# Kernel optimization log

Hardware: AMD Instinct MI355X
Metric: run time of the kernel (lower is better)

## Reference

```python
import jax, jax.numpy as jnp
import numpy as np

LMAX, MMAX = 4, 2
K = (LMAX + 1) ** 2                                 # 25 SH coefficients (l-major node layout)
NL = [LMAX - m + 1 for m in range(MMAX + 1)]        # coeffs per order m: [5,4,3]
M_COEFF = NL[0] + sum(2 * n for n in NL[1:])        # 19 coeffs in m-major (mmax-truncated) edge layout
SPHERE_C, HIDDEN_C = 64, 64
NUM_HEADS, ALPHA_C, VALUE_C, OUT_C = 8, 32, 16, 64
P_GRID = 100
N_NODES, N_EDGES = 4096, 24576
NUM_SPECIES, EDGE_C, EMB_C = 90, 64, 64
N_EXTRA = NUM_HEADS * ALPHA_C + HIDDEN_C            # extra m=0 channels for S2_SEP: alpha + gate scalars


def _ln(x, g, b, eps=1e-5):
    mu = jnp.mean(x, -1, keepdims=True)
    var = jnp.var(x, -1, keepdims=True)
    return (x - mu) * jax.lax.rsqrt(var + eps) * g + b


def _smooth_leaky_relu(x, neg=0.2):
    return 0.5 * (1.0 + neg) * x + 0.5 * (1.0 - neg) * x * (2.0 * jax.nn.sigmoid(x) - 1.0)


def _segment_softmax(a, seg, n):
    amax = jax.lax.stop_gradient(jax.ops.segment_max(a, seg, num_segments=n))
    amax = jnp.where(jnp.isfinite(amax), amax, 0.0)
    e = jnp.exp(a - amax[seg])
    s = jax.ops.segment_sum(e, seg, num_segments=n)
    return e / (s[seg] + 1e-16)


def _so2_conv(x, w0, b0, wms, c_in, c_out, x_edge=None, n_extra=0):
    # x: [E, M_COEFF, c_in] in m-major layout (m=0 block, then per m: real rows then imag rows)
    E = x.shape[0]
    L0 = NL[0]
    x0 = x[:, :L0, :].reshape(E, L0 * c_in)
    if x_edge is not None:
        x0 = x0 * x_edge[:, :L0 * c_in]
    y0 = x0 @ w0 + b0
    extra = None
    if n_extra:
        extra = y0[:, L0 * c_out:]
        y0 = y0[:, :L0 * c_out]
    outs = [y0.reshape(E, L0, c_out)]
    off, rad = L0, L0 * c_in
    for m in range(1, MMAX + 1):
        nl = NL[m]
        xr = x[:, off:off + nl, :]
        xi = x[:, off + nl:off + 2 * nl, :]
        if x_edge is not None:
            s = x_edge[:, rad:rad + nl * c_in].reshape(E, nl, c_in)
            xr, xi = xr * s, xi * s
        xr = xr.reshape(E, nl * c_in)
        xi = xi.reshape(E, nl * c_in)
        half = nl * c_out
        wa, wb = wms[m - 1][:, :half], wms[m - 1][:, half:]
        yr = (xr @ wa - xi @ wb).reshape(E, nl, c_out)  # complex block-matmul
        yi = (xr @ wb + xi @ wa).reshape(E, nl, c_out)
        outs.append(jnp.concatenate([yr, yi], axis=1))
        off += 2 * nl
        rad += nl * c_in
    return jnp.concatenate(outs, axis=1), extra


def setup_inputs():
    key = jax.random.key(0)
    ks = iter(jax.random.split(key, 48))
    def w(shape, fan_in):
        return jax.random.normal(next(ks), shape, jnp.float32) / np.sqrt(fan_in)
    inp = {}
    inp['node_feats'] = jax.random.normal(next(ks), (N_NODES, K, SPHERE_C), jnp.float32)
    inp['node_species'] = jax.random.randint(next(ks), (N_NODES,), 0, NUM_SPECIES)
    inp['edge_distances'] = jax.random.normal(next(ks), (N_EDGES, EDGE_C), jnp.float32)
    inp['senders'] = jax.random.randint(next(ks), (N_EDGES,), 0, N_NODES)
    inp['receivers'] = jax.random.randint(next(ks), (N_EDGES,), 0, N_NODES)
    inp['wigner'] = jax.random.normal(next(ks), (N_EDGES, M_COEFF, K), jnp.float32) / np.sqrt(K)
    inp['snd_emb'] = jax.random.normal(next(ks), (NUM_SPECIES, EMB_C), jnp.float32) * 0.001
    inp['rcv_emb'] = jax.random.normal(next(ks), (NUM_SPECIES, EMB_C), jnp.float32) * 0.001
    ec = EDGE_C + 2 * EMB_C                              # 192 after atom-edge embedding concat
    n_rad = 2 * SPHERE_C * (NL[0] + NL[1] + NL[2])       # 1536 per-edge scales for conv1
    inp['rad_w1'] = w((ec, 64), ec); inp['rad_b1'] = jnp.zeros((64,))
    inp['rad_g1'] = jnp.ones((64,)); inp['rad_be1'] = jnp.zeros((64,))
    inp['rad_w2'] = w((64, 64), 64); inp['rad_b2'] = jnp.zeros((64,))
    inp['rad_g2'] = jnp.ones((64,)); inp['rad_be2'] = jnp.zeros((64,))
    inp['rad_w3'] = w((64, n_rad), 64); inp['rad_b3'] = jnp.ones((n_rad,))
    cin1 = 2 * SPHERE_C
    inp['c1_w0'] = w((NL[0] * cin1, NL[0] * HIDDEN_C + N_EXTRA), NL[0] * cin1)
    inp['c1_b0'] = jnp.zeros((NL[0] * HIDDEN_C + N_EXTRA,))
    inp['c1_wm1'] = w((NL[1] * cin1, 2 * NL[1] * HIDDEN_C), NL[1] * cin1)
    inp['c1_wm2'] = w((NL[2] * cin1, 2 * NL[2] * HIDDEN_C), NL[2] * cin1)
    inp['aln_g'] = jnp.ones((ALPHA_C,)); inp['aln_b'] = jnp.zeros((ALPHA_C,))
    inp['alpha_dot'] = w((NUM_HEADS, ALPHA_C), ALPHA_C)
    inp['to_grid'] = jax.random.normal(next(ks), (P_GRID, M_COEFF), jnp.float32) / np.sqrt(M_COEFF)
    inp['from_grid'] = jax.random.normal(next(ks), (M_COEFF, P_GRID), jnp.float32) / np.sqrt(P_GRID)
    cv = NUM_HEADS * VALUE_C
    inp['c2_w0'] = w((NL[0] * HIDDEN_C, NL[0] * cv), NL[0] * HIDDEN_C)
    inp['c2_b0'] = jnp.zeros((NL[0] * cv,))
    inp['c2_wm1'] = w((NL[1] * HIDDEN_C, 2 * NL[1] * cv), NL[1] * HIDDEN_C)
    inp['c2_wm2'] = w((NL[2] * HIDDEN_C, 2 * NL[2] * cv), NL[2] * HIDDEN_C)
    inp['proj_w'] = w((LMAX + 1, cv, OUT_C), cv)
    inp['proj_b'] = jnp.zeros((OUT_C,))
    return inp


def reference(node_feats, node_species, edge_distances, senders, receivers, wigner,
              snd_emb, rcv_emb, rad_w1, rad_b1, rad_g1, rad_be1, rad_w2, rad_b2,
              rad_g2, rad_be2, rad_w3, rad_b3, c1_w0, c1_b0, c1_wm1, c1_wm2,
              aln_g, aln_b, alpha_dot, to_grid, from_grid,
              c2_w0, c2_b0, c2_wm1, c2_wm2, proj_w, proj_b):
    N = node_feats.shape[0]
    # atom-edge embedding gathers + concat with radial-basis distances
    edge_embeds = jnp.concatenate([edge_distances,
                                   snd_emb[node_species[senders]],
                                   rcv_emb[node_species[receivers]]], axis=1)
    msgs = jnp.concatenate([node_feats[senders], node_feats[receivers]], axis=2)  # [E,25,128]
    msgs = jnp.einsum('emk,ekc->emc', wigner, msgs)                               # rotate to edge frame [E,19,128]
    # radial function -> per-edge input scales for SO2 conv 1
    h = jax.nn.silu(_ln(edge_embeds @ rad_w1 + rad_b1, rad_g1, rad_be1))
    h = jax.nn.silu(_ln(h @ rad_w2 + rad_b2, rad_g2, rad_be2))
    x_edge = h @ rad_w3 + rad_b3
    msgs, x0_extra = _so2_conv(msgs, c1_w0, c1_b0, [c1_wm1, c1_wm2],
                               2 * SPHERE_C, HIDDEN_C, x_edge, N_EXTRA)
    x0_alpha = x0_extra[:, :NUM_HEADS * ALPHA_C]
    x0_gate = x0_extra[:, NUM_HEADS * ALPHA_C:]
    # separable S2 activation: SiLU on sphere grid for l>0, SiLU on scalars for l=0
    grid = jax.nn.silu(jnp.einsum('pm,emc->epc', to_grid, msgs))
    tens = jnp.einsum('mp,epc->emc', from_grid, grid)
    msgs = jnp.concatenate([jax.nn.silu(x0_gate)[:, None, :], tens[:, 1:, :]], axis=1)
    msgs, _ = _so2_conv(msgs, c2_w0, c2_b0, [c2_wm1, c2_wm2], HIDDEN_C, NUM_HEADS * VALUE_C)
    # attention weights: LN -> SmoothLeakyReLU -> dot -> per-receiver softmax
    a = _smooth_leaky_relu(_ln(x0_alpha.reshape(-1, NUM_HEADS, ALPHA_C), aln_g, aln_b))
    alpha = _segment_softmax(jnp.einsum('ehk,hk->eh', a, alpha_dot), receivers, N)
    attn = msgs.reshape(-1, M_COEFF, NUM_HEADS, VALUE_C) * alpha[:, None, :, None]
    msgs = attn.reshape(-1, M_COEFF, NUM_HEADS * VALUE_C)
    msgs = jnp.einsum('emk,emc->ekc', wigner, msgs)    # rotate back (W^T), [E,25,128]
    node = jax.ops.segment_sum(msgs, receivers, num_segments=N)
    # SO3 linear: per-degree-l channel mixing, bias only on l=0
    l_of_k = jnp.asarray(np.repeat(np.arange(LMAX + 1), 2 * np.arange(LMAX + 1) + 1))
    out = jnp.einsum('nkc,kcd->nkd', node, proj_w[l_of_k])
    return out.at[:, 0, :].add(proj_b)
```

## Files before the change

kernel.cpp:

```cpp
#include <hip/hip_runtime.h>

typedef unsigned short u16;
typedef unsigned int u32;
typedef __attribute__((ext_vector_type(8))) short short8;
typedef __attribute__((ext_vector_type(4))) float floatx4;

#define E_EDGES 24576
#define EC 12288
#define N_NODES_C 4096

__device__ __forceinline__ float bf2f(u16 u) {
    union { u32 i; float f; } v; v.i = ((u32)u) << 16; return v.f;
}
__device__ __forceinline__ u16 f2bf(float f) {
    union { float f; u32 i; } v; v.f = f;
    u32 x = v.i;
    u32 r = (x + 0x7fffu + ((x >> 16) & 1u)) >> 16;
    return (u16)r;
}
__device__ __forceinline__ u32 pk_bf16(float a, float b) {
    u32 r;
    asm("v_cvt_pk_bf16_f32 %0, %1, %2" : "=v"(r) : "v"(a), "v"(b));
    return r;
}
__device__ __forceinline__ u32 encf(float f) {
    union { float f; u32 i; } v; v.f = f;
    return (v.i & 0x80000000u) ? ~v.i : (v.i | 0x80000000u);
}
__device__ __forceinline__ float decf(u32 u) {
    union { u32 i; float f; } v;
    v.i = (u & 0x80000000u) ? (u ^ 0x80000000u) : ~u;
    return v.f;
}
__device__ __forceinline__ float sigmoidf_(float x) { return __fdividef(1.f, 1.f + __expf(-x)); }
__device__ __forceinline__ float siluf_(float x) { return x * __fdividef(1.f, 1.f + __expf(-x)); }

__device__ __forceinline__ void gld16(const u16* g, u16* l) {
    __builtin_amdgcn_global_load_lds((const __attribute__((address_space(1))) unsigned int*)g,
                                     (__attribute__((address_space(3))) unsigned int*)l, 16, 0, 0);
}

__global__ void k_diag(float* __restrict__ out, int n) {
    int i = blockIdx.x * 256 + threadIdx.x;
    if (i < n) out[i] = 1000.0f;
}

__global__ void k_transpose(const float* __restrict__ src, u16* __restrict__ dst, int K, int N) {
    int idx = blockIdx.x * 256 + threadIdx.x;
    if (idx >= K * N) return;
    int k = idx / N, n = idx % N;
    dst[n * K + k] = f2bf(src[idx]);
}
__global__ void k_combine(const float* __restrict__ src, u16* __restrict__ dst, int K, int H) {
    int total = 4 * K * H;
    int idx = blockIdx.x * 256 + threadIdx.x;
    if (idx >= total) return;
    int n = idx / (2 * K), k = idx % (2 * K);
    float v;
    if (k < K) v = src[k * 2 * H + n];
    else {
        int kk = k - K;
        if (n < H) v = -src[kk * 2 * H + H + n];
        else       v = src[kk * 2 * H + (n - H)];
    }
    dst[idx] = f2bf(v);
}

__global__ void k_packgrid(const float* __restrict__ tg, const float* __restrict__ fg,
                           u16* __restrict__ tgP, u16* __restrict__ fgP) {
    int idx = blockIdx.x * 256 + threadIdx.x;
    if (idx < 112 * 32) {
        int p = idx >> 5, m = idx & 31;
        tgP[idx] = (p < 100 && m < 19) ? f2bf(tg[p * 19 + m]) : (u16)0;
    }
    int j = idx - 112 * 32;
    if (j >= 0 && j < 32 * 128) {
        int m = j >> 7, k = j & 127;
        fgP[j] = (m < 19 && k < 100) ? f2bf(fg[m * 100 + k]) : (u16)0;
    }
}

__global__ void k_init(u32* __restrict__ nmax, float* __restrict__ nsum, int n) {
    int idx = blockIdx.x * 256 + threadIdx.x;
    if (idx < n) { nmax[idx] = 0x007FFFFFu;  nsum[idx] = 0.f; }
}

__global__ void k_deg(const int* __restrict__ rcv, u32* __restrict__ deg) {
    int e = blockIdx.x * 256 + threadIdx.x;
    if (e < E_EDGES) atomicAdd(&deg[rcv[e]], 1u);
}
__global__ __launch_bounds__(256) void k_pfx(const u32* __restrict__ deg,
                                             u32* __restrict__ rowstart, u32* __restrict__ cur) {
    __shared__ u32 ps[256];
    int t = threadIdx.x;
    u32 loc[16]; u32 s = 0;
#pragma unroll
    for (int i = 0; i < 16; i++) { loc[i] = s; s += deg[t * 16 + i]; }
    ps[t] = s;
    __syncthreads();
    for (int o = 1; o < 256; o <<= 1) {
        u32 v = (t >= o) ? ps[t - o] : 0u;
        __syncthreads();
        ps[t] += v;
        __syncthreads();
    }
    u32 base = (t == 0) ? 0u : ps[t - 1];
#pragma unroll
    for (int i = 0; i < 16; i++) { u32 v = base + loc[i]; rowstart[t * 16 + i] = v; cur[t * 16 + i] = v; }
}
__global__ void k_fill(const int* __restrict__ rcv, u32* __restrict__ cur, int* __restrict__ elist) {
    int e = blockIdx.x * 256 + threadIdx.x;
    if (e < E_EDGES) { u32 p = atomicAdd(&cur[rcv[e]], 1u); elist[p] = e; }
}

__global__ void k_ee(const float* __restrict__ dist, const int* __restrict__ species,
                     const int* __restrict__ snd, const int* __restrict__ rcv,
                     const float* __restrict__ semb, const float* __restrict__ remb,
                     u16* __restrict__ ee) {
    int idx = blockIdx.x * 256 + threadIdx.x;
    if (idx >= E_EDGES * 192) return;
    int e = idx / 192, c = idx % 192;
    float v;
    if (c < 64)       v = dist[e * 64 + c];
    else if (c < 128) v = semb[species[snd[e]] * 64 + (c - 64)];
    else              v = remb[species[rcv[e]] * 64 + (c - 128)];
    ee[idx] = f2bf(v);
}

__global__ __launch_bounds__(256) void k_gemm(
    const u16* __restrict__ A, int lda,
    const u16* __restrict__ BT, int ldb,
    u16* __restrict__ C, int ldc,
    int N, int K,
    const float* __restrict__ bias) {
    __shared__ u16 As[128 * 32];
    __shared__ u16 Bs[128 * 32];
    int tid = threadIdx.x;
    int bm0 = blockIdx.x * 128;
    int bn0 = blockIdx.y * 128;
    int wave = tid >> 6, lane = tid & 63;
    int wm = (wave >> 1) * 64, wn = (wave & 1) * 64;
    int lrow = lane & 15, lk = (lane >> 4) * 8;

    int srow = (wave << 4) + (lane >> 2);
    int schunk = (lane & 3) << 3;
    const u16* Arow0 = A + (size_t)(bm0 + srow) * lda + schunk;
    const u16* Arow1 = A + (size_t)(bm0 + srow + 64) * lda + schunk;
    int n0 = bn0 + srow;      if (n0 >= N) n0 = N - 1;
    int n1 = bn0 + srow + 64; if (n1 >= N) n1 = N - 1;
    const u16* Brow0 = BT + (size_t)n0 * ldb + schunk;
    const u16* Brow1 = BT + (size_t)n1 * ldb + schunk;
    u16* lA0 = &As[srow * 32 + schunk];
    u16* lA1 = &As[(srow + 64) * 32 + schunk];
    u16* lB0 = &Bs[srow * 32 + schunk];
    u16* lB1 = &Bs[(srow + 64) * 32 + schunk];

    floatx4 acc[4][4];
#pragma unroll
    for (int i = 0; i < 4; i++)
#pragma unroll
        for (int j = 0; j < 4; j++) acc[i][j] = floatx4{0.f, 0.f, 0.f, 0.f};

    for (int k0 = 0; k0 < K; k0 += 32) {
        gld16(Arow0 + k0, lA0);
        gld16(Arow1 + k0, lA1);
        gld16(Brow0 + k0, lB0);
        gld16(Brow1 + k0, lB1);
        asm volatile("s_waitcnt vmcnt(0)" ::: "memory");
        __syncthreads();
        short8 a[4], b[4];
#pragma unroll
        for (int i = 0; i < 4; i++) a[i] = *(const short8*)(&As[(wm + i * 16 + lrow) * 32 + lk]);
#pragma unroll
        for (int j = 0; j < 4; j++) b[j] = *(const short8*)(&Bs[(wn + j * 16 + lrow) * 32 + lk]);
#pragma unroll
        for (int i = 0; i < 4; i++)
#pragma unroll
            for (int j = 0; j < 4; j++)
                acc[i][j] = __builtin_amdgcn_mfma_f32_16x16x32_bf16(b[j], a[i], acc[i][j], 0, 0, 0);
        __syncthreads();
    }

    int q = lane >> 4;
#pragma unroll
    for (int i = 0; i < 4; i++) {
        int row = bm0 + wm + i * 16 + lrow;
#pragma unroll
        for (int j = 0; j < 4; j++) {
            int col = bn0 + wn + j * 16 + q * 4;
            if (col < N) {
                float4 bv = bias ? *(const float4*)(&bias[col]) : float4{0.f, 0.f, 0.f, 0.f};
                uint2 pv;
                pv.x = pk_bf16(acc[i][j][0] + bv.x, acc[i][j][1] + bv.y);
                pv.y = pk_bf16(acc[i][j][2] + bv.z, acc[i][j][3] + bv.w);
                *(uint2*)(&C[(size_t)row * ldc + col]) = pv;
            }
        }
    }
}

__global__ __launch_bounds__(256) void k_ln_silu(const u16* __restrict__ in, u16* __restrict__ out,
                                                 const float* __restrict__ g, const float* __restrict__ b) {
    int tid = threadIdx.x;
    int e = blockIdx.x * 4 + (tid >> 6);
    int c = tid & 63;
    float x = bf2f(in[(size_t)e * 64 + c]);
    float s = x, s2 = x * x;
#pragma unroll
    for (int o = 32; o; o >>= 1) { s += __shfl_xor(s, o); s2 += __shfl_xor(s2, o); }
    float mu = s * (1.f / 64.f);
    float var = s2 * (1.f / 64.f) - mu * mu;
    float rs = rsqrtf(var + 1e-5f);
    float y = (x - mu) * rs * g[c] + b[c];
    out[(size_t)e * 64 + c] = f2bf(siluf_(y));
}

__global__ __launch_bounds__(256) void k_rotate(const float* __restrict__ nf, const float* __restrict__ wig,
                                                const int* __restrict__ snd, const int* __restrict__ rcv,
                                                const u16* __restrict__ xe, u16* __restrict__ A1, int e0) {
    __shared__ float wl[2][475];
    int tid = threadIdx.x;
    for (int i = tid; i < 950; i += 256) {
        int ee = e0 + blockIdx.x * 2 + (i / 475);
        wl[i / 475][i % 475] = wig[(size_t)ee * 475 + (i % 475)];
    }
    __syncthreads();
    int le = tid >> 7, c = tid & 127;
    int el = blockIdx.x * 2 + le;
    int e = e0 + el;
    int nd = (c < 64) ? snd[e] : rcv[e];
    int cc = c & 63;
    float msg[25];
#pragma unroll
    for (int k = 0; k < 25; k++) msg[k] = nf[(size_t)nd * 1600 + k * 64 + cc];
    const float* w = wl[le];
    size_t ebase = (size_t)el * 2432;
    size_t xbase = (size_t)el * 1536;
#pragma unroll
    for (int m = 0; m < 19; m++) {
        float r = 0.f;
#pragma unroll
        for (int k = 0; k < 25; k++) r += w[m * 25 + k] * msg[k];
        int a1c, xc;
        if (m < 5)       { a1c = m * 128;               xc = m * 128; }
        else if (m < 9)  { a1c = 640 + (m - 5) * 128;   xc = 640 + (m - 5) * 128; }
        else if (m < 13) { a1c = 1152 + (m - 9) * 128;  xc = 640 + (m - 9) * 128; }
        else if (m < 16) { a1c = 1664 + (m - 13) * 128; xc = 1152 + (m - 13) * 128; }
        else             { a1c = 2048 + (m - 16) * 128; xc = 1152 + (m - 16) * 128; }
        float sc = bf2f(xe[xbase + xc + c]);
        A1[ebase + a1c + c] = f2bf(r * sc);
    }
}

__global__ __launch_bounds__(256) void k_logits(const u16* __restrict__ Y0, const int* __restrict__ rcv,
                                                const float* __restrict__ g, const float* __restrict__ b,
                                                const float* __restrict__ adot,
                                                float* __restrict__ logits, u32* __restrict__ nmax) {
    int e = blockIdx.x;
    int tid = threadIdx.x;
    int h = tid >> 5, c = tid & 31;
    float x = bf2f(Y0[(size_t)e * 640 + 320 + h * 32 + c]);
    float s = x, s2 = x * x;
#pragma unroll
    for (int o = 16; o; o >>= 1) { s += __shfl_xor(s, o); s2 += __shfl_xor(s2, o); }
    float mu = s * (1.f / 32.f);
    float var = s2 * (1.f / 32.f) - mu * mu;
    float rs = rsqrtf(var + 1e-5f);
    float a = (x - mu) * rs * g[c] + b[c];
    float f = 0.6f * a + 0.4f * a * (2.f * sigmoidf_(a) - 1.f);
    float l = f * adot[h * 32 + c];
#pragma unroll
    for (int o = 16; o; o >>= 1) l += __shfl_xor(l, o);
    if (c == 0) {
        logits[e * 8 + h] = l;
        atomicMax(&nmax[rcv[e] * 8 + h], encf(l));
    }
}

__global__ void k_expsum(const float* __restrict__ logits, const int* __restrict__ rcv,
                         const u32* __restrict__ nmax, float* __restrict__ ealpha, float* __restrict__ nsum) {
    int idx = blockIdx.x * 256 + threadIdx.x;
    if (idx >= E_EDGES * 8) return;
    int e = idx >> 3, h = idx & 7;
    int r = rcv[e];
    float amax = decf(nmax[r * 8 + h]);
    if (!(amax > -1e38f && amax < 1e38f)) amax = 0.f;
    float v = __expf(logits[idx] - amax);
    ealpha[idx] = v;
    atomicAdd(&nsum[r * 8 + h], v);
}

#define GR_XS_STR 40
#define GR_T1_STR 136
__global__ __launch_bounds__(256) void k_grid_mfma(
    const u16* __restrict__ Y0, const u16* __restrict__ Y1, const u16* __restrict__ Y2,
    const u16* __restrict__ tgP, const u16* __restrict__ fgP, u16* __restrict__ A2) {
    __shared__ u16 T1s[128 * GR_T1_STR];
    u16* Xs = T1s;
    int tid = threadIdx.x;
    int e0 = blockIdx.x * 2;
    {
        int mp = tid & 15;
        int c0 = ((tid >> 4) & 7) << 3;
        int le = tid >> 7;
        int e = e0 + le;
        int m0 = 2 * mp, m1 = m0 + 1;
        uint4 va = {0, 0, 0, 0}, vb = {0, 0, 0, 0};
        if (m0 < 5)       va = *(const uint4*)(&Y0[(size_t)e * 640 + m0 * 64 + c0]);
        else if (m0 < 13) va = *(const uint4*)(&Y1[(size_t)e * 512 + (m0 - 5) * 64 + c0]);
        else if (m0 < 19) va = *(const uint4*)(&Y2[(size_t)e * 384 + (m0 - 13) * 64 + c0]);
        if (m1 < 5)       vb = *(const uint4*)(&Y0[(size_t)e * 640 + m1 * 64 + c0]);
        else if (m1 < 13) vb = *(const uint4*)(&Y1[(size_t)e * 512 + (m1 - 5) * 64 + c0]);
        else if (m1 < 19) vb = *(const uint4*)(&Y2[(size_t)e * 384 + (m1 - 13) * 64 + c0]);
        const u16* pa = (const u16*)&va;
        const u16* pb = (const u16*)&vb;
        int rbase = le * 64 + c0;
#pragma unroll
        for (int j = 0; j < 8; j++) {
            u32 w = (u32)pa[j] | ((u32)pb[j] << 16);
            *(u32*)(&Xs[(rbase + j) * GR_XS_STR + 2 * mp]) = w;
        }
    }
    __syncthreads();
    int wave = tid >> 6, lane = tid & 63;
    int wn = wave << 5;
    int ln = lane & 15, q = lane >> 4;
    short8 bx0 = *(const short8*)(&Xs[(wn + ln) * GR_XS_STR + q * 8]);
    short8 bx1 = *(const short8*)(&Xs[(wn + 16 + ln) * GR_XS_STR + q * 8]);
    floatx4 acc1[2][7];
#pragma unroll
    for (int pt = 0; pt < 7; pt++) {
        short8 a = *(const short8*)(&tgP[(size_t)(pt * 16 + ln) * 32 + q * 8]);
        acc1[0][pt] = __builtin_amdgcn_mfma_f32_16x16x32_bf16(a, bx0, floatx4{0.f, 0.f, 0.f, 0.f}, 0, 0, 0);
        acc1[1][pt] = __builtin_amdgcn_mfma_f32_16x16x32_bf16(a, bx1, floatx4{0.f, 0.f, 0.f, 0.f}, 0, 0, 0);
    }
    __syncthreads();
    {
        int row = tid >> 1;
        uint4 z = {0, 0, 0, 0};
        *(uint4*)(&T1s[row * GR_T1_STR + 112 + (tid & 1) * 8]) = z;
    }
#pragma unroll
    for (int i = 0; i < 2; i++) {
        u16* dst = &T1s[(wn + i * 16 + ln) * GR_T1_STR + q * 4];
#pragma unroll
        for (int pt = 0; pt < 7; pt++) {
            uint2 pv;
            pv.x = pk_bf16(siluf_(acc1[i][pt][0]), siluf_(acc1[i][pt][1]));
            pv.y = pk_bf16(siluf_(acc1[i][pt][2]), siluf_(acc1[i][pt][3]));
            *(uint2*)(dst + pt * 16) = pv;
        }
    }
    __syncthreads();
    floatx4 acc2[2][2];
    acc2[0][0] = floatx4{0.f, 0.f, 0.f, 0.f}; acc2[0][1] = floatx4{0.f, 0.f, 0.f, 0.f};
    acc2[1][0] = floatx4{0.f, 0.f, 0.f, 0.f}; acc2[1][1] = floatx4{0.f, 0.f, 0.f, 0.f};
#pragma unroll
    for (int ks = 0; ks < 4; ks++) {
        short8 c0 = *(const short8*)(&T1s[(wn + ln) * GR_T1_STR + ks * 32 + q * 8]);
        short8 c1 = *(const short8*)(&T1s[(wn + 16 + ln) * GR_T1_STR + ks * 32 + q * 8]);
#pragma unroll
        for (int ct = 0; ct < 2; ct++) {
            short8 b = *(const short8*)(&fgP[(size_t)(ct * 16 + ln) * 128 + ks * 32 + q * 8]);
            acc2[0][ct] = __builtin_amdgcn_mfma_f32_16x16x32_bf16(c0, b, acc2[0][ct], 0, 0, 0);
            acc2[1][ct] = __builtin_amdgcn_mfma_f32_16x16x32_bf16(c1, b, acc2[1][ct], 0, 0, 0);
        }
    }
#pragma unroll
    for (int rt = 0; rt < 2; rt++) {
        int row = wn + rt * 16 + q * 4;
        int e = e0 + (row >> 6), c = row & 63;
#pragma unroll
        for (int ct = 0; ct < 2; ct++) {
            int mp = ct * 16 + ln;
            if (mp >= 1 && mp < 19) {
                uint2 pv;
                pv.x = pk_bf16(acc2[rt][ct][0], acc2[rt][ct][1]);
                pv.y = pk_bf16(acc2[rt][ct][2], acc2[rt][ct][3]);
                *(uint2*)(&A2[(size_t)e * 1216 + mp * 64 + c]) = pv;
            }
        }
    }
    if (tid < 128) {
        int e = e0 + (tid >> 6), c = tid & 63;
        float gate = bf2f(Y0[(size_t)e * 640 + 576 + c]);
        A2[(size_t)e * 1216 + c] = f2bf(siluf_(gate));
    }
}

__global__ __launch_bounds__(256) void k_gather(
    const u16* __restrict__ Z0, const u16* __restrict__ Z1, const u16* __restrict__ Z2,
    const float* __restrict__ wig, const float* __restrict__ ealpha, const float* __restrict__ nsum,
    const u32* __restrict__ rowstart, const u32* __restrict__ deg, const int* __restrict__ elist,
    float* __restrict__ node, int e0, int accum) {
    int n = blockIdx.x * 4 + (threadIdx.x >> 6);
    int lane = threadIdx.x & 63;
    int h = lane >> 3;
    float sden = __fdividef(1.f, nsum[n * 8 + h] + 1e-16f);
    float a0[25], a1[25];
#pragma unroll
    for (int k = 0; k < 25; k++) { a0[k] = 0.f; a1[k] = 0.f; }
    u32 lo = rowstart[n], cnt = deg[n];
    bool did = false;
    for (u32 i = 0; i < cnt; i++) {
        int e = __builtin_amdgcn_readfirstlane(elist[lo + i]);
        int el = e - e0;
        if ((u32)el >= (u32)EC) continue;
        did = true;
        float al = ealpha[e * 8 + h] * sden;
        u32 zp[19];
        const u16* z0 = Z0 + (size_t)el * 640 + 2 * lane;
        const u16* z1 = Z1 + (size_t)el * 1024 + 2 * lane;
        const u16* z2 = Z2 + (size_t)el * 768 + 2 * lane;
#pragma unroll
        for (int m = 0; m < 5; m++) zp[m] = *(const u32*)(z0 + m * 128);
#pragma unroll
        for (int m = 0; m < 8; m++) zp[5 + m] = *(const u32*)(z1 + m * 128);
#pragma unroll
        for (int m = 0; m < 6; m++) zp[13 + m] = *(const u32*)(z2 + m * 128);
        const float* __restrict__ w = wig + (size_t)e * 475;
#pragma unroll
        for (int m = 0; m < 19; m++) {
            float s0 = bf2f((u16)(zp[m] & 0xffffu)) * al;
            float s1 = bf2f((u16)(zp[m] >> 16)) * al;
#pragma unroll
            for (int k = 0; k < 25; k++) {
                float wv = w[m * 25 + k];
                a0[k] = fmaf(wv, s0, a0[k]);
                a1[k] = fmaf(wv, s1, a1[k]);
            }
        }
    }
    float* nb = node + (size_t)n * 3200 + 2 * lane;
    if (accum) {
        if (!did) return;
#pragma unroll
        for (int k = 0; k < 25; k++) {
            float2 v = *(float2*)(&nb[k * 128]);
            v.x += a0[k]; v.y += a1[k];
            *(float2*)(&nb[k * 128]) = v;
        }
    } else {
#pragma unroll
        for (int k = 0; k < 25; k++) {
            float2 v; v.x = a0[k]; v.y = a1[k];
            *(float2*)(&nb[k * 128]) = v;
        }
    }
}

#define PJ_STR 136
__global__ __launch_bounds__(256) void k_proj_mfma(
    const float* __restrict__ node, const u16* __restrict__ pwTb,
    const float* __restrict__ pb, float* __restrict__ out) {
    __shared__ u16 As[128 * PJ_STR];
    __shared__ u16 Bs[64 * PJ_STR];
    int tid = threadIdx.x;
    int n0 = blockIdx.x * 128;
    int k = blockIdx.y;
    int l = (int)sqrtf((float)k + 0.5f);
#pragma unroll
    for (int it = 0; it < 16; it++) {
        int i = tid + it * 256;
        int row = i >> 5;
        int c0 = (i & 31) << 2;
        float4 v = *(const float4*)(&node[(size_t)(n0 + row) * 3200 + k * 128 + c0]);
        uint2 pv;
        pv.x = pk_bf16(v.x, v.y);
        pv.y = pk_bf16(v.z, v.w);
        *(uint2*)(&As[row * PJ_STR + c0]) = pv;
    }
    const u16* pw = pwTb + (size_t)l * 8192;
#pragma unroll
    for (int jt = 0; jt < 4; jt++) {
        int j = tid + jt * 256;
        int d = j >> 4;
        int c0 = (j & 15) << 3;
        *(uint4*)(&Bs[d * PJ_STR + c0]) = *(const uint4*)(&pw[d * 128 + c0]);
    }
    __syncthreads();
    int wave = tid >> 6, lane = tid & 63;
    int wr = wave * 32;
    int ln = lane & 15, q = lane >> 4;
    floatx4 acc[2][4];
#pragma unroll
    for (int i = 0; i < 2; i++)
#pragma unroll
        for (int j = 0; j < 4; j++) acc[i][j] = floatx4{0.f, 0.f, 0.f, 0.f};
#pragma unroll
    for (int ks = 0; ks < 4; ks++) {
        short8 a0 = *(const short8*)(&As[(wr + ln) * PJ_STR + ks * 32 + q * 8]);
        short8 a1 = *(const short8*)(&As[(wr + 16 + ln) * PJ_STR + ks * 32 + q * 8]);
#pragma unroll
        for (int j = 0; j < 4; j++) {
            short8 b = *(const short8*)(&Bs[(j * 16 + ln) * PJ_STR + ks * 32 + q * 8]);
            acc[0][j] = __builtin_amdgcn_mfma_f32_16x16x32_bf16(b, a0, acc[0][j], 0, 0, 0);
            acc[1][j] = __builtin_amdgcn_mfma_f32_16x16x32_bf16(b, a1, acc[1][j], 0, 0, 0);
        }
    }
#pragma unroll
    for (int rt = 0; rt < 2; rt++) {
        int n = n0 + wr + rt * 16 + ln;
#pragma unroll
        for (int j = 0; j < 4; j++) {
            int d = j * 16 + q * 4;
            float4 v;
            v.x = acc[rt][j][0]; v.y = acc[rt][j][1];
            v.z = acc[rt][j][2]; v.w = acc[rt][j][3];
            if (k == 0) {
                float4 bv = *(const float4*)(&pb[d]);
                v.x += bv.x; v.y += bv.y; v.z += bv.z; v.w += bv.w;
            }
            *(float4*)(&out[(size_t)n * 1600 + k * 64 + d]) = v;
        }
    }
}

extern "C" void kernel_launch(void* const* d_in, const int* in_sizes, int n_in,
                              void* d_out, int out_size, void* d_ws, size_t ws_size,
                              hipStream_t stream) {
    const float* nf      = (const float*)d_in[0];
    const int* species   = (const int*)d_in[1];
    const float* dist    = (const float*)d_in[2];
    const int* snd       = (const int*)d_in[3];
    const int* rcv       = (const int*)d_in[4];
    const float* wig     = (const float*)d_in[5];
    const float* semb    = (const float*)d_in[6];
    const float* remb    = (const float*)d_in[7];
    const float* rad_w1  = (const float*)d_in[8];
    const float* rad_b1  = (const float*)d_in[9];
    const float* rad_g1  = (const float*)d_in[10];
    const float* rad_be1 = (const float*)d_in[11];
    const float* rad_w2  = (const float*)d_in[12];
    const float* rad_b2  = (const float*)d_in[13];
    const float* rad_g2  = (const float*)d_in[14];
    const float* rad_be2 = (const float*)d_in[15];
    const float* rad_w3  = (const float*)d_in[16];
    const float* rad_b3  = (const float*)d_in[17];
    const float* c1_w0   = (const float*)d_in[18];
    const float* c1_b0   = (const float*)d_in[19];
    const float* c1_wm1  = (const float*)d_in[20];
    const float* c1_wm2  = (const float*)d_in[21];
    const float* aln_g   = (const float*)d_in[22];
    const float* aln_b   = (const float*)d_in[23];
    const float* adot    = (const float*)d_in[24];
    const float* to_grid = (const float*)d_in[25];
    const float* from_grid=(const float*)d_in[26];
    const float* c2_w0   = (const float*)d_in[27];
    const float* c2_b0   = (const float*)d_in[28];
    const float* c2_wm1  = (const float*)d_in[29];
    const float* c2_wm2  = (const float*)d_in[30];
    const float* proj_w  = (const float*)d_in[31];
    const float* proj_b  = (const float*)d_in[32];

    char* ws = (char*)d_ws;
    size_t off = 0;
    auto take = [&](size_t bytes) -> char* {
        char* p = ws + off;
        off += (bytes + 255) & ~(size_t)255;
        return p;
    };
    u16* w_rad1T  = (u16*)take(64 * 192 * 2);
    u16* w_rad2T  = (u16*)take(64 * 64 * 2);
    u16* w_rad3T  = (u16*)take(1536 * 64 * 2);
    u16* w_c1w0T  = (u16*)take(640 * 640 * 2);
    u16* w_c1m1T  = (u16*)take((size_t)512 * 1024 * 2);
    u16* w_c1m2T  = (u16*)take((size_t)384 * 768 * 2);
    u16* w_c2w0T  = (u16*)take((size_t)640 * 320 * 2);
    u16* w_c2m1T  = (u16*)take((size_t)1024 * 512 * 2);
    u16* w_c2m2T  = (u16*)take((size_t)768 * 384 * 2);
    u16* w_tgP    = (u16*)take(112 * 32 * 2);
    u16* w_fgP    = (u16*)take(32 * 128 * 2);
    u16* w_pwT    = (u16*)take(5 * 8192 * 2);
    float* logits = (float*)take((size_t)E_EDGES * 8 * 4);
    float* ealpha = (float*)take((size_t)E_EDGES * 8 * 4);
    u32* nmax     = (u32*)take((size_t)N_NODES_C * 8 * 4);
    float* nsum   = (float*)take((size_t)N_NODES_C * 8 * 4);
    float* node   = (float*)take((size_t)N_NODES_C * 3200 * 4);
    u16* a_h2     = (u16*)take((size_t)E_EDGES * 64 * 2);
    u32* c_deg    = (u32*)take((size_t)N_NODES_C * 4);
    u32* c_row    = (u32*)take((size_t)N_NODES_C * 4);
    u32* c_cur    = (u32*)take((size_t)N_NODES_C * 4);
    int* c_elist  = (int*)take((size_t)E_EDGES * 4);
    char* arena   = take(173015040);
    if (off > ws_size) {
        k_diag<<<(out_size + 255) / 256, 256, 0, stream>>>((float*)d_out, out_size);
        return;
    }

    u16* a_ee   = (u16*)(arena + 0);
    u16* a_ypre = (u16*)(arena + 9437184);
    u16* a_h1   = (u16*)(arena + 12582912);
    u16* a_xe   = (u16*)(arena + 0);
    u16* a_A1   = (u16*)(arena + 37748736);
    u16* a_Y0   = (u16*)(arena + 97517568);
    u16* a_Y1   = (u16*)(arena + 128974848);
    u16* a_Y2   = (u16*)(arena + 154140672);
    u16* a_A2   = (u16*)(arena + 0);
    u16* a_Z0   = (u16*)(arena + 59768832);
    u16* a_Z1   = (u16*)(arena + 75497472);
    u16* a_Z2   = (u16*)(arena + 100663296);

    k_transpose<<<48, 256, 0, stream>>>(rad_w1, w_rad1T, 192, 64);
    k_transpose<<<16, 256, 0, stream>>>(rad_w2, w_rad2T, 64, 64);
    k_transpose<<<384, 256, 0, stream>>>(rad_w3, w_rad3T, 64, 1536);
    k_transpose<<<1600, 256, 0, stream>>>(c1_w0, w_c1w0T, 640, 640);
    k_transpose<<<800, 256, 0, stream>>>(c2_w0, w_c2w0T, 320, 640);
    k_combine<<<2048, 256, 0, stream>>>(c1_wm1, w_c1m1T, 512, 256);
    k_combine<<<1152, 256, 0, stream>>>(c1_wm2, w_c1m2T, 384, 192);
    k_combine<<<2048, 256, 0, stream>>>(c2_wm1, w_c2m1T, 256, 512);
    k_combine<<<1152, 256, 0, stream>>>(c2_wm2, w_c2m2T, 192, 384);
    k_packgrid<<<30, 256, 0, stream>>>(to_grid, from_grid, w_tgP, w_fgP);
    for (int l = 0; l < 5; l++)
        k_transpose<<<32, 256, 0, stream>>>(proj_w + (size_t)l * 8192, w_pwT + (size_t)l * 8192, 128, 64);
    k_init<<<128, 256, 0, stream>>>(nmax, nsum, N_NODES_C * 8);

    hipMemsetAsync(c_deg, 0, (size_t)N_NODES_C * 4, stream);
    k_deg<<<96, 256, 0, stream>>>(rcv, c_deg);
    k_pfx<<<1, 256, 0, stream>>>(c_deg, c_row, c_cur);
    k_fill<<<96, 256, 0, stream>>>(rcv, c_cur, c_elist);

    k_ee<<<(E_EDGES * 192 + 255) / 256, 256, 0, stream>>>(dist, species, snd, rcv, semb, remb, a_ee);
    k_gemm<<<dim3(192, 1), 256, 0, stream>>>(a_ee, 192, w_rad1T, 192, a_ypre, 64, 64, 192, rad_b1);
    k_ln_silu<<<6144, 256, 0, stream>>>(a_ypre, a_h1, rad_g1, rad_be1);
    k_gemm<<<dim3(192, 1), 256, 0, stream>>>(a_h1, 64, w_rad2T, 64, a_ypre, 64, 64, 64, rad_b2);
    k_ln_silu<<<6144, 256, 0, stream>>>(a_ypre, a_h2, rad_g2, rad_be2);

    for (int c = 0; c < 2; c++) {
        int e0 = c * EC;
        k_gemm<<<dim3(96, 12), 256, 0, stream>>>(a_h2 + (size_t)e0 * 64, 64, w_rad3T, 64,
                                                 a_xe, 1536, 1536, 64, rad_b3);
        k_rotate<<<EC / 2, 256, 0, stream>>>(nf, wig, snd, rcv, a_xe, a_A1, e0);
        k_gemm<<<dim3(96, 5), 256, 0, stream>>>(a_A1, 2432, w_c1w0T, 640,
                                                a_Y0 + (size_t)e0 * 640, 640, 640, 640, c1_b0);
        k_gemm<<<dim3(96, 4), 256, 0, stream>>>(a_A1 + 640, 2432, w_c1m1T, 1024,
                                                a_Y1 + (size_t)e0 * 512, 512, 512, 1024, nullptr);
        k_gemm<<<dim3(96, 3), 256, 0, stream>>>(a_A1 + 1664, 2432, w_c1m2T, 768,
                                                a_Y2 + (size_t)e0 * 384, 384, 384, 768, nullptr);
    }

    k_logits<<<E_EDGES, 256, 0, stream>>>(a_Y0, rcv, aln_g, aln_b, adot, logits, nmax);
    k_expsum<<<(E_EDGES * 8 + 255) / 256, 256, 0, stream>>>(logits, rcv, nmax, ealpha, nsum);

    k_grid_mfma<<<E_EDGES / 2, 256, 0, stream>>>(a_Y0, a_Y1, a_Y2, w_tgP, w_fgP, a_A2);

    for (int c = 0; c < 2; c++) {
        int e0 = c * EC;
        k_gemm<<<dim3(96, 5), 256, 0, stream>>>(a_A2 + (size_t)e0 * 1216, 1216, w_c2w0T, 320,
                                                a_Z0, 640, 640, 320, c2_b0);
        k_gemm<<<dim3(96, 8), 256, 0, stream>>>(a_A2 + (size_t)e0 * 1216 + 320, 1216, w_c2m1T, 512,
                                                a_Z1, 1024, 1024, 512, nullptr);
        k_gemm<<<dim3(96, 6), 256, 0, stream>>>(a_A2 + (size_t)e0 * 1216 + 832, 1216, w_c2m2T, 384,
                                                a_Z2, 768, 768, 384, nullptr);
        k_gather<<<N_NODES_C / 4, 256, 0, stream>>>(a_Z0, a_Z1, a_Z2, wig, ealpha, nsum,
                                                    c_row, c_deg, c_elist, node, e0, c);
    }

    k_proj_mfma<<<dim3(32, 25), 256, 0, stream>>>(node, w_pwT, proj_b, (float*)d_out);
}
```

Before: 1.027 ms.

## Double-buffer LDS tiles in GEMM to overlap global loads with MFMA

Gives the bf16 MFMA GEMM kernel two LDS buffers for the A and B tiles. The next K-slice's global-to-LDS loads are issued before computing on the current slice, and the wait is relaxed to vmcnt(4) so the in-flight prefetch is not waited on. This hides global memory latency behind matrix compute, at the cost of doubling shared memory per block, which can reduce occupancy.

```diff
diff --git a/kernel.cpp b/kernel.cpp
--- a/kernel.cpp
+++ b/kernel.cpp
@@ -133,8 +133,8 @@
     u16* __restrict__ C, int ldc,
     int N, int K,
     const float* __restrict__ bias) {
-    __shared__ u16 As[128 * 32];
-    __shared__ u16 Bs[128 * 32];
+    __shared__ u16 As[2][128 * 32];
+    __shared__ u16 Bs[2][128 * 32];
     int tid = threadIdx.x;
     int bm0 = blockIdx.x * 128;
     int bn0 = blockIdx.y * 128;
@@ -150,10 +150,13 @@
     int n1 = bn0 + srow + 64; if (n1 >= N) n1 = N - 1;
     const u16* Brow0 = BT + (size_t)n0 * ldb + schunk;
     const u16* Brow1 = BT + (size_t)n1 * ldb + schunk;
-    u16* lA0 = &As[srow * 32 + schunk];
-    u16* lA1 = &As[(srow + 64) * 32 + schunk];
-    u16* lB0 = &Bs[srow * 32 + schunk];
-    u16* lB1 = &Bs[(srow + 64) * 32 + schunk];
+
+    auto stage = [&](int buf, int k0) {
+        gld16(Arow0 + k0, &As[buf][srow * 32 + schunk]);
+        gld16(Arow1 + k0, &As[buf][(srow + 64) * 32 + schunk]);
+        gld16(Brow0 + k0, &Bs[buf][srow * 32 + schunk]);
+        gld16(Brow1 + k0, &Bs[buf][(srow + 64) * 32 + schunk]);
+    };
 
     floatx4 acc[4][4];
 #pragma unroll
@@ -161,18 +164,22 @@
 #pragma unroll
         for (int j = 0; j < 4; j++) acc[i][j] = floatx4{0.f, 0.f, 0.f, 0.f};
 
-    for (int k0 = 0; k0 < K; k0 += 32) {
-        gld16(Arow0 + k0, lA0);
-        gld16(Arow1 + k0, lA1);
-        gld16(Brow0 + k0, lB0);
-        gld16(Brow1 + k0, lB1);
-        asm volatile("s_waitcnt vmcnt(0)" ::: "memory");
+    int NT = K >> 5;
+    stage(0, 0);
+    for (int kt = 0; kt < NT; kt++) {
+        int cur = kt & 1;
+        if (kt + 1 < NT) {
+            stage(cur ^ 1, (kt + 1) << 5);
+            asm volatile("s_waitcnt vmcnt(4)" ::: "memory");
+        } else {
+            asm volatile("s_waitcnt vmcnt(0)" ::: "memory");
+        }
         __syncthreads();
         short8 a[4], b[4];
 #pragma unroll
-        for (int i = 0; i < 4; i++) a[i] = *(const short8*)(&As[(wm + i * 16 + lrow) * 32 + lk]);
-#pragma unroll
-        for (int j = 0; j < 4; j++) b[j] = *(const short8*)(&Bs[(wn + j * 16 + lrow) * 32 + lk]);
+        for (int i = 0; i < 4; i++) a[i] = *(const short8*)(&As[cur][(wm + i * 16 + lrow) * 32 + lk]);
+#pragma unroll
+        for (int j = 0; j < 4; j++) b[j] = *(const short8*)(&Bs[cur][(wn + j * 16 + lrow) * 32 + lk]);
 #pragma unroll
         for (int i = 0; i < 4; i++)
 #pragma unroll
```

Result: no change. 1.016 ms (-1.0%).
